# Optimization experiments

Measured on AMD Instinct MI355X. Metric: run time of the kernel, lower is better.

Reference implementation:

```python
import jax, jax.numpy as jnp
import numpy as np

B, C, M, H, K, V = 2, 2048, 1024, 16, 64, 64


def setup_inputs() -> dict:
    key = jax.random.key(0)
    ks = jax.random.split(key, 6)
    mscale = 1.0 / np.sqrt(M)
    vscale = 1.0 / np.sqrt(V)
    return {
        "kvinput": jax.random.normal(ks[0], (B, C, M), dtype=jnp.float32),
        "qinput": jax.random.normal(ks[1], (B, C, M), dtype=jnp.float32),
        "wq": jax.random.normal(ks[2], (H, M, K), dtype=jnp.float32) * mscale,
        "wk": jax.random.normal(ks[3], (H, M, K), dtype=jnp.float32) * mscale,
        "wv": jax.random.normal(ks[4], (H, M, V), dtype=jnp.float32) * mscale,
        "wo": jax.random.normal(ks[5], (H, V, M), dtype=jnp.float32) * vscale,
    }


def reference(kvinput, qinput, wq, wk, wv, wo):
    scale = 1.0 / np.sqrt(K).astype(np.float32)
    kval = jnp.einsum('bcm,hmk->bhck', kvinput, wk)
    qval = jnp.einsum('bcm,hmk->bhck', qinput, wq)
    vval = jnp.einsum('bcm,hmv->bhcv', kvinput, wv)
    # NOTE: c indexes keys, d indexes queries (faithful to the original einsum order)
    alogit = jnp.einsum('bhck,bhdk->bhcd', kval, qval)
    # additive -100 mask on strictly-lower triangle (key pos c > query pos d), as in source
    mask = jnp.tri(alogit.shape[2], k=-1, dtype=alogit.dtype) * -100.0
    alogit = alogit + mask
    att = jax.nn.softmax(alogit * scale, axis=2)  # softmax over key axis c
    pre = jnp.einsum('bhcd,bhcv->bhdv', att, vval)
    out = jnp.einsum('bhcv,hvm->bcm', pre, wo)
    return out
```

## Files before the change

### kernel.cpp

```cpp
#include <hip/hip_runtime.h>
#include <hip/hip_bf16.h>

typedef __bf16 bf16;
typedef __attribute__((ext_vector_type(8))) __bf16 bf16x8;
typedef __attribute__((ext_vector_type(4))) __bf16 bf16x4;
typedef __attribute__((ext_vector_type(4))) float f32x4;

#define NB 2
#define NC 2048
#define NM 1024
#define NH 16
#define NK 64
#define NV 64
#define NHV 1024

#define MFMA(a, b, c) __builtin_amdgcn_mfma_f32_16x16x32_bf16((a), (b), (c), 0, 0, 0)

__device__ const unsigned char J8[8][4] = {
  {0, 4, 12, 19},
  {31, 1, 13, 21},
  {30, 2, 14, 20},
  {29, 3, 15, 18},
  {28, 5, 16, 17},
  {27, 6, 11, 22},
  {26, 7, 10, 23},
  {25, 8, 9, 24},
};

__global__ __launch_bounds__(256) void prep_kernel(
    const float* __restrict__ qin, const float* __restrict__ kvin,
    const float* __restrict__ wq, const float* __restrict__ wk,
    const float* __restrict__ wv, const float* __restrict__ wo,
    bf16* __restrict__ qb, bf16* __restrict__ kvb,
    bf16* __restrict__ wqT, bf16* __restrict__ wkT,
    bf16* __restrict__ wvT, bf16* __restrict__ woT) {
  __shared__ float tile[32][33];
  const int bx = blockIdx.x;
  const int tid = threadIdx.x;
  if (bx < 1024) {
    const float4* src = (const float4*)((bx < 512) ? qin : kvin);
    bf16x4* dst = (bf16x4*)((bx < 512) ? qb : kvb);
    int base = (bx & 511) * 2048;
#pragma unroll
    for (int k = 0; k < 8; ++k) {
      int i = base + k * 256 + tid;
      float4 v = src[i];
      bf16x4 o;
      o.x = (bf16)v.x; o.y = (bf16)v.y; o.z = (bf16)v.z; o.w = (bf16)v.w;
      dst[i] = o;
    }
  } else if (bx < 4096) {
    const int sel = (bx >> 10) - 1;
    const float* w = (sel == 0) ? wq : (sel == 1) ? wk : wv;
    bf16* wT = (sel == 0) ? wqT : (sel == 1) ? wkT : wvT;
    const int t = bx & 1023;
    const int k0 = (t & 1) * 32, m0 = ((t >> 1) & 31) * 32, h = t >> 6;
    const int tx = tid & 31, ty = tid >> 5;
#pragma unroll
    for (int dy = 0; dy < 32; dy += 8)
      tile[ty + dy][tx] = w[((size_t)h * NM + m0 + ty + dy) * NK + k0 + tx];
    __syncthreads();
#pragma unroll
    for (int dy = 0; dy < 32; dy += 8)
      wT[((size_t)h * NK + k0 + ty + dy) * NM + m0 + tx] = (bf16)tile[tx][ty + dy];
  } else {
    const int t = bx & 1023;
    const int hv0 = (t & 31) * 32, m0 = (t >> 5) * 32;
    const int tx = tid & 31, ty = tid >> 5;
#pragma unroll
    for (int dy = 0; dy < 32; dy += 8)
      tile[ty + dy][tx] = wo[((size_t)(hv0 + ty + dy)) * NM + m0 + tx];
    __syncthreads();
#pragma unroll
    for (int dy = 0; dy < 32; dy += 8)
      woT[((size_t)(m0 + ty + dy)) * NHV + hv0 + tx] = (bf16)tile[tx][ty + dy];
  }
}

__global__ __launch_bounds__(256, 6) void proj_fused_kernel(
    const bf16* __restrict__ qb, const bf16* __restrict__ kvb,
    const bf16* __restrict__ wqT, const bf16* __restrict__ wkT,
    const bf16* __restrict__ wvT, bf16* __restrict__ Qp,
    bf16* __restrict__ Kp, bf16* __restrict__ VpT) {
  __shared__ bf16 Al[128 * 64], Bl[64 * 64];
  const int z = blockIdx.z;
  const bf16* Ain = (z == 0) ? qb : kvb;
  const bf16* BTin = (z == 0) ? wqT : (z == 1) ? wkT : wvT;
  const int m0 = blockIdx.x * 128, n0 = blockIdx.y * 64;
  const int tid = threadIdx.x;
  const int w = tid >> 6, lane = tid & 63, lr = lane & 15, lg = lane >> 4;
  const int wm = w >> 1, wn = w & 1;
  f32x4 acc[4][2] = {};
  for (int k0 = 0; k0 < 1024; k0 += 64) {
#pragma unroll
    for (int it = 0; it < 4; ++it) {
      int id = it * 256 + tid;
      int row = id >> 3, ch = (id & 7) ^ (row & 7);
      __builtin_amdgcn_global_load_lds(
          (const __attribute__((address_space(1))) void*)(Ain +
              (size_t)(m0 + row) * 1024 + k0 + ch * 8),
          (__attribute__((address_space(3))) void*)&Al[(it * 256 + w * 64) * 8],
          16, 0, 0);
    }
#pragma unroll
    for (int it = 0; it < 2; ++it) {
      int id = it * 256 + tid;
      int row = id >> 3, ch = (id & 7) ^ (row & 7);
      __builtin_amdgcn_global_load_lds(
          (const __attribute__((address_space(1))) void*)(BTin +
              (size_t)(n0 + row) * 1024 + k0 + ch * 8),
          (__attribute__((address_space(3))) void*)&Bl[(it * 256 + w * 64) * 8],
          16, 0, 0);
    }
    __syncthreads();
#pragma unroll
    for (int ks = 0; ks < 2; ++ks) {
      bf16x8 a[4], bb[2];
#pragma unroll
      for (int i = 0; i < 4; ++i) {
        int ra = wm * 64 + i * 16 + lr;
        a[i] = *reinterpret_cast<const bf16x8*>(
            &Al[ra * 64 + (((ks * 4 + lg) ^ (ra & 7)) << 3)]);
      }
#pragma unroll
      for (int i = 0; i < 2; ++i) {
        int rb = wn * 32 + i * 16 + lr;
        bb[i] = *reinterpret_cast<const bf16x8*>(
            &Bl[rb * 64 + (((ks * 4 + lg) ^ (rb & 7)) << 3)]);
      }
#pragma unroll
      for (int mi = 0; mi < 4; ++mi)
#pragma unroll
        for (int ni = 0; ni < 2; ++ni)
          acc[mi][ni] = MFMA(a[mi], bb[ni], acc[mi][ni]);
    }
    __syncthreads();
  }
  if (z < 2) {
    bf16* dst = (z == 0) ? Qp : Kp;
#pragma unroll
    for (int mi = 0; mi < 4; ++mi)
#pragma unroll
      for (int ni = 0; ni < 2; ++ni)
#pragma unroll
        for (int j = 0; j < 4; ++j) {
          int gm = m0 + wm * 64 + mi * 16 + 4 * lg + j;
          int gn = n0 + wn * 32 + ni * 16 + lr;
          dst[(((size_t)((gm >> 11) * 16 + (gn >> 6)) * 2048 + (gm & 2047)) << 6) +
              (gn & 63)] = (bf16)acc[mi][ni][j];
        }
  } else {
#pragma unroll
    for (int mi = 0; mi < 4; ++mi)
#pragma unroll
      for (int ni = 0; ni < 2; ++ni) {
        int gm0 = m0 + wm * 64 + mi * 16 + 4 * lg;
        int gn = n0 + wn * 32 + ni * 16 + lr;
        bf16x4 pv;
#pragma unroll
        for (int j = 0; j < 4; ++j) pv[j] = (bf16)acc[mi][ni][j];
        *reinterpret_cast<bf16x4*>(
            &VpT[((size_t)((gm0 >> 11) * 16 + (gn >> 6)) * 64 + (gn & 63)) * 2048 +
                 (gm0 & 2047)]) = pv;
      }
  }
}

__global__ __launch_bounds__(256) void out_gemm_kernel(
    const bf16* __restrict__ preb, const bf16* __restrict__ woT,
    float* __restrict__ out) {
  __shared__ bf16 Al[64 * 64], Bl[128 * 64];
  const int m0 = blockIdx.x * 64, n0 = blockIdx.y * 128;
  const int tid = threadIdx.x;
  const int w = tid >> 6, lane = tid & 63, lr = lane & 15, lg = lane >> 4;
  const int wm = w >> 1, wn = w & 1;
  f32x4 acc[2][4] = {};
  for (int k0 = 0; k0 < 1024; k0 += 64) {
#pragma unroll
    for (int it = 0; it < 2; ++it) {
      int id = it * 256 + tid;
      int row = id >> 3, ch = (id & 7) ^ (row & 7);
      __builtin_amdgcn_global_load_lds(
          (const __attribute__((address_space(1))) void*)(preb +
              (size_t)(m0 + row) * 1024 + k0 + ch * 8),
          (__attribute__((address_space(3))) void*)&Al[(it * 256 + w * 64) * 8],
          16, 0, 0);
    }
#pragma unroll
    for (int it = 0; it < 4; ++it) {
      int id = it * 256 + tid;
      int row = id >> 3, ch = (id & 7) ^ (row & 7);
      __builtin_amdgcn_global_load_lds(
          (const __attribute__((address_space(1))) void*)(woT +
              (size_t)(n0 + row) * 1024 + k0 + ch * 8),
          (__attribute__((address_space(3))) void*)&Bl[(it * 256 + w * 64) * 8],
          16, 0, 0);
    }
    __syncthreads();
#pragma unroll
    for (int ks = 0; ks < 2; ++ks) {
      bf16x8 a[2], bb[4];
#pragma unroll
      for (int i = 0; i < 2; ++i) {
        int ra = wm * 32 + i * 16 + lr;
        a[i] = *reinterpret_cast<const bf16x8*>(
            &Al[ra * 64 + (((ks * 4 + lg) ^ (ra & 7)) << 3)]);
      }
#pragma unroll
      for (int i = 0; i < 4; ++i) {
        int rb = wn * 64 + i * 16 + lr;
        bb[i] = *reinterpret_cast<const bf16x8*>(
            &Bl[rb * 64 + (((ks * 4 + lg) ^ (rb & 7)) << 3)]);
      }
#pragma unroll
      for (int mi = 0; mi < 2; ++mi)
#pragma unroll
        for (int ni = 0; ni < 4; ++ni)
          acc[mi][ni] = MFMA(a[mi], bb[ni], acc[mi][ni]);
    }
    __syncthreads();
  }
#pragma unroll
  for (int mi = 0; mi < 2; ++mi)
#pragma unroll
    for (int ni = 0; ni < 4; ++ni)
#pragma unroll
      for (int j = 0; j < 4; ++j) {
        int gm = m0 + wm * 32 + mi * 16 + 4 * lg + j;
        int gn = n0 + wn * 64 + ni * 16 + lr;
        out[(size_t)gm * 1024 + gn] = acc[mi][ni][j];
      }
}

__global__ __launch_bounds__(256) void attn_kernel(
    const bf16* __restrict__ Qp, const bf16* __restrict__ Kp,
    const bf16* __restrict__ VpT, bf16* __restrict__ preb) {
  __shared__ bf16 Klds[2][64 * 64];
  __shared__ bf16 Vlds[2][64 * 64];
  __shared__ bf16 Plds[4][16 * 64];

  const int g = blockIdx.x;
  const int c = (g >> 3) & 31;
  const int bh = 4 * (g & 7) + (c & 3);
  const int j = J8[c >> 2][g >> 8];
  const int b = bh >> 4, h = bh & 15;
  const int tid = threadIdx.x;
  const int w = tid >> 6;
  const int lane = tid & 63;
  const int lr = lane & 15, lg = lane >> 4;
  const int qb0 = j * 64 + w * 16;

  const bf16* Qb = Qp + (size_t)bh * NC * NK;
  const bf16* Kb = Kp + (size_t)bh * NC * NK;
  const bf16* Vb = VpT + (size_t)bh * NV * NC;
  char* PL = (char*)&Plds[w][0];

  bf16x8 qfr[2];
#pragma unroll
  for (int s = 0; s < 2; ++s)
    qfr[s] = *reinterpret_cast<const bf16x8*>(
        Qb + (size_t)(qb0 + lr) * NK + s * 32 + lg * 8);

  f32x4 acc[4] = {};
  float llane = 0.f;

  const float M0 = 8.0f;
  const float MK = -12.5f;

  const int srow = tid >> 3;
  const int sch0 = tid & 7;
  auto STAGE = [&](int buf, int c0) {
#pragma unroll
    for (int i = 0; i < 2; ++i) {
      int row = i * 32 + srow;
      int ch = sch0 ^ (row & 7);
      __builtin_amdgcn_global_load_lds(
          (const __attribute__((address_space(1))) void*)(
              Kb + (size_t)(c0 + row) * NK + ch * 8),
          (__attribute__((address_space(3))) void*)&Klds[buf][(i * 32 + w * 8) * 64],
          16, 0, 0);
      __builtin_amdgcn_global_load_lds(
          (const __attribute__((address_space(1))) void*)(
              Vb + (size_t)row * NC + c0 + ch * 8),
          (__attribute__((address_space(3))) void*)&Vlds[buf][(i * 32 + w * 8) * 64],
          16, 0, 0);
    }
  };

  const int nt = (j == 0) ? (NC / 64) : (j + 1);

  STAGE(0, 0);
  asm volatile("s_waitcnt vmcnt(0)" ::: "memory");
  __syncthreads();

  for (int t = 0; t < nt; ++t) {
    const int cur = t & 1;
    const int c0 = t * 64;
    if (t + 1 < nt) STAGE(cur ^ 1, (t + 1) * 64);

    const char* KL = (const char*)&Klds[cur][0];
    const char* VL = (const char*)&Vlds[cur][0];

    f32x4 S[4] = {};
#pragma unroll
    for (int s = 0; s < 2; ++s)
#pragma unroll
      for (int kf = 0; kf < 4; ++kf) {
        bf16x8 kfr = *reinterpret_cast<const bf16x8*>(
            KL + (kf * 16 + lr) * 128 + (((s * 4 + lg) ^ (lr & 7)) << 4));
        S[kf] = MFMA(kfr, qfr[s], S[kf]);
      }

    {
      const int qg = qb0 + lr;
      bf16x4 pq[4];
      if (t < j) {
#pragma unroll
        for (int kf = 0; kf < 4; ++kf)
#pragma unroll
          for (int i = 0; i < 4; ++i) {
            float p = __expf(fmaf(S[kf][i], 0.125f, -M0));
            llane += p;
            pq[kf][i] = (bf16)p;
          }
      } else if (t == j) {
#pragma unroll
        for (int kf = 0; kf < 4; ++kf)
#pragma unroll
          for (int i = 0; i < 4; ++i) {
            int key = c0 + kf * 16 + 4 * lg + i;
            float off = (key > qg) ? (MK - M0) : -M0;
            float p = __expf(fmaf(S[kf][i], 0.125f, off));
            llane += p;
            pq[kf][i] = (bf16)p;
          }
      } else {
#pragma unroll
        for (int kf = 0; kf < 4; ++kf)
#pragma unroll
          for (int i = 0; i < 4; ++i) {
            float p = __expf(fmaf(S[kf][i], 0.125f, MK - M0));
            llane += p;
            pq[kf][i] = (bf16)p;
          }
      }
#pragma unroll
      for (int kf = 0; kf < 4; ++kf) {
        int cc = 2 * kf + (lg >> 1);
        *reinterpret_cast<bf16x4*>(
            PL + lr * 128 + ((cc ^ (lr & 7)) << 4) + (lg & 1) * 8) = pq[kf];
      }
    }

#pragma unroll
    for (int s2 = 0; s2 < 2; ++s2) {
      bf16x8 pa = *reinterpret_cast<const bf16x8*>(
          PL + lr * 128 + (((s2 * 4 + lg) ^ (lr & 7)) << 4));
#pragma unroll
      for (int vf = 0; vf < 4; ++vf) {
        bf16x8 vfr = *reinterpret_cast<const bf16x8*>(
            VL + (vf * 16 + lr) * 128 + (((s2 * 4 + lg) ^ (lr & 7)) << 4));
        acc[vf] = MFMA(pa, vfr, acc[vf]);
      }
    }

    asm volatile("s_waitcnt vmcnt(0)" ::: "memory");
    __syncthreads();
  }

  llane += __shfl_xor(llane, 16);
  llane += __shfl_xor(llane, 32);
  float li[4];
#pragma unroll
  for (int i = 0; i < 4; ++i) li[i] = 1.0f / __shfl(llane, 4 * lg + i);
  bf16* ob = preb + ((size_t)b * NC) * NHV + (size_t)h * NV;
#pragma unroll
  for (int vf = 0; vf < 4; ++vf)
#pragma unroll
    for (int i = 0; i < 4; ++i) {
      int d = qb0 + 4 * lg + i;
      ob[(size_t)d * NHV + vf * 16 + lr] = (bf16)(acc[vf][i] * li[i]);
    }
}


extern "C" void kernel_launch(void* const* d_in, const int* in_sizes, int n_in,
                              void* d_out, int out_size, void* d_ws, size_t ws_size,
                              hipStream_t stream) {
  const float* kvinput = (const float*)d_in[0];
  const float* qinput  = (const float*)d_in[1];
  const float* wq = (const float*)d_in[2];
  const float* wk = (const float*)d_in[3];
  const float* wv = (const float*)d_in[4];
  const float* wo = (const float*)d_in[5];
  float* out = (float*)d_out;

  char* ws = (char*)d_ws;
  bf16* qb   = (bf16*)(ws + 0);
  bf16* kvb  = (bf16*)(ws + 8388608);
  bf16* wqT  = (bf16*)(ws + 16777216);
  bf16* wkT  = (bf16*)(ws + 18874368);
  bf16* wvT  = (bf16*)(ws + 20971520);
  bf16* woT  = (bf16*)(ws + 23068672);
  bf16* Qp   = (bf16*)(ws + 25165824);
  bf16* Kp   = (bf16*)(ws + 33554432);
  bf16* VpT  = (bf16*)(ws + 41943040);
  bf16* preb = (bf16*)(ws + 50331648);

  prep_kernel<<<5120, 256, 0, stream>>>(qinput, kvinput, wq, wk, wv, wo,
                                        qb, kvb, wqT, wkT, wvT, woT);

  dim3 pg(32, 16, 3);
  proj_fused_kernel<<<pg, 256, 0, stream>>>(qb, kvb, wqT, wkT, wvT, Qp, Kp, VpT);

  attn_kernel<<<1024, 256, 0, stream>>>(Qp, Kp, VpT, preb);

  dim3 og(64, 8);
  out_gemm_kernel<<<og, 256, 0, stream>>>(preb, woT, out);
}
```

Before: 116.9 us.

## Double-buffer LDS in projection GEMM and widen tile to 128x128

The projection GEMM now stages the next K-slice into a second LDS buffer while MFMAs run on the current one, removing the serialized load-then-compute pattern. The output tile per block grows from 128x64 to 128x128 (each wave computes 4x4 MFMA tiles), so the grid halves in the N dimension and A-tile reuse improves. In exchange, LDS use rises to 64KB per block and register pressure grows, and the occupancy hint is dropped, so fewer blocks will be resident per CU. With only 768 blocks there is also less parallelism to hide latency.

Result: faster. 107.7 us (-7.8%).

```diff
diff --git a/kernel.cpp b/kernel.cpp
--- a/kernel.cpp
+++ b/kernel.cpp
@@ -77,75 +77,83 @@
   }
 }
 
-__global__ __launch_bounds__(256, 6) void proj_fused_kernel(
+__global__ __launch_bounds__(256) void proj_fused_kernel(
     const bf16* __restrict__ qb, const bf16* __restrict__ kvb,
     const bf16* __restrict__ wqT, const bf16* __restrict__ wkT,
     const bf16* __restrict__ wvT, bf16* __restrict__ Qp,
     bf16* __restrict__ Kp, bf16* __restrict__ VpT) {
-  __shared__ bf16 Al[128 * 64], Bl[64 * 64];
+  __shared__ bf16 Al[2][128 * 64], Bl[2][128 * 64];
   const int z = blockIdx.z;
   const bf16* Ain = (z == 0) ? qb : kvb;
   const bf16* BTin = (z == 0) ? wqT : (z == 1) ? wkT : wvT;
-  const int m0 = blockIdx.x * 128, n0 = blockIdx.y * 64;
+  const int m0 = blockIdx.x * 128, n0 = blockIdx.y * 128;
   const int tid = threadIdx.x;
   const int w = tid >> 6, lane = tid & 63, lr = lane & 15, lg = lane >> 4;
   const int wm = w >> 1, wn = w & 1;
-  f32x4 acc[4][2] = {};
-  for (int k0 = 0; k0 < 1024; k0 += 64) {
+  f32x4 acc[4][4] = {};
+
+  const int srow = tid >> 3;
+  const int sch0 = tid & 7;
+  auto STAGE = [&](int buf, int k0) {
 #pragma unroll
     for (int it = 0; it < 4; ++it) {
-      int id = it * 256 + tid;
-      int row = id >> 3, ch = (id & 7) ^ (row & 7);
+      int row = it * 32 + srow;
+      int ch = sch0 ^ (row & 7);
       __builtin_amdgcn_global_load_lds(
           (const __attribute__((address_space(1))) void*)(Ain +
               (size_t)(m0 + row) * 1024 + k0 + ch * 8),
-          (__attribute__((address_space(3))) void*)&Al[(it * 256 + w * 64) * 8],
-          16, 0, 0);
-    }
-#pragma unroll
-    for (int it = 0; it < 2; ++it) {
-      int id = it * 256 + tid;
-      int row = id >> 3, ch = (id & 7) ^ (row & 7);
+          (__attribute__((address_space(3))) void*)&Al[buf][(it * 256 + w * 64) * 8],
+          16, 0, 0);
       __builtin_amdgcn_global_load_lds(
           (const __attribute__((address_space(1))) void*)(BTin +
               (size_t)(n0 + row) * 1024 + k0 + ch * 8),
-          (__attribute__((address_space(3))) void*)&Bl[(it * 256 + w * 64) * 8],
-          16, 0, 0);
-    }
-    __syncthreads();
+          (__attribute__((address_space(3))) void*)&Bl[buf][(it * 256 + w * 64) * 8],
+          16, 0, 0);
+    }
+  };
+
+  STAGE(0, 0);
+  asm volatile("s_waitcnt vmcnt(0)" ::: "memory");
+  __syncthreads();
+
+  int cur = 0;
+  for (int k0 = 0; k0 < 1024; k0 += 64) {
+    if (k0 + 64 < 1024) STAGE(cur ^ 1, k0 + 64);
+    const bf16* AL = &Al[cur][0];
+    const bf16* BL = &Bl[cur][0];
 #pragma unroll
     for (int ks = 0; ks < 2; ++ks) {
-      bf16x8 a[4], bb[2];
+      bf16x8 a[4], bb[4];
 #pragma unroll
       for (int i = 0; i < 4; ++i) {
         int ra = wm * 64 + i * 16 + lr;
         a[i] = *reinterpret_cast<const bf16x8*>(
-            &Al[ra * 64 + (((ks * 4 + lg) ^ (ra & 7)) << 3)]);
-      }
-#pragma unroll
-      for (int i = 0; i < 2; ++i) {
-        int rb = wn * 32 + i * 16 + lr;
+            &AL[ra * 64 + (((ks * 4 + lg) ^ (ra & 7)) << 3)]);
+        int rb = wn * 64 + i * 16 + lr;
         bb[i] = *reinterpret_cast<const bf16x8*>(
-            &Bl[rb * 64 + (((ks * 4 + lg) ^ (rb & 7)) << 3)]);
+            &BL[rb * 64 + (((ks * 4 + lg) ^ (rb & 7)) << 3)]);
       }
 #pragma unroll
       for (int mi = 0; mi < 4; ++mi)
 #pragma unroll
-        for (int ni = 0; ni < 2; ++ni)
+        for (int ni = 0; ni < 4; ++ni)
           acc[mi][ni] = MFMA(a[mi], bb[ni], acc[mi][ni]);
     }
-    __syncthreads();
+    asm volatile("s_waitcnt vmcnt(0)" ::: "memory");
+    __syncthreads();
+    cur ^= 1;
   }
+
   if (z < 2) {
     bf16* dst = (z == 0) ? Qp : Kp;
 #pragma unroll
     for (int mi = 0; mi < 4; ++mi)
 #pragma unroll
-      for (int ni = 0; ni < 2; ++ni)
+      for (int ni = 0; ni < 4; ++ni)
 #pragma unroll
         for (int j = 0; j < 4; ++j) {
           int gm = m0 + wm * 64 + mi * 16 + 4 * lg + j;
-          int gn = n0 + wn * 32 + ni * 16 + lr;
+          int gn = n0 + wn * 64 + ni * 16 + lr;
           dst[(((size_t)((gm >> 11) * 16 + (gn >> 6)) * 2048 + (gm & 2047)) << 6) +
               (gn & 63)] = (bf16)acc[mi][ni][j];
         }
@@ -153,9 +161,9 @@
 #pragma unroll
     for (int mi = 0; mi < 4; ++mi)
 #pragma unroll
-      for (int ni = 0; ni < 2; ++ni) {
+      for (int ni = 0; ni < 4; ++ni) {
         int gm0 = m0 + wm * 64 + mi * 16 + 4 * lg;
-        int gn = n0 + wn * 32 + ni * 16 + lr;
+        int gn = n0 + wn * 64 + ni * 16 + lr;
         bf16x4 pv;
 #pragma unroll
         for (int j = 0; j < 4; ++j) pv[j] = (bf16)acc[mi][ni][j];
@@ -410,7 +418,7 @@
   prep_kernel<<<5120, 256, 0, stream>>>(qinput, kvinput, wq, wk, wv, wo,
                                         qb, kvb, wqT, wkT, wvT, woT);
 
-  dim3 pg(32, 16, 3);
+  dim3 pg(32, 8, 3);
   proj_fused_kernel<<<pg, 256, 0, stream>>>(qb, kvb, wqT, wkT, wvT, Qp, Kp, VpT);
 
   attn_kernel<<<1024, 256, 0, stream>>>(Qp, Kp, VpT, preb);
```
